# Performance work log

Measured on AMD Instinct MI355X. Metric: run time of the kernel, lower is better.

Reference implementation:

```python
import jax, jax.numpy as jnp
import numpy as np

N_NODES = 100000
D_MODEL = 256
N_SLOTS = 512


def setup_inputs() -> dict:
    key = jax.random.key(0)
    k1, k2, k3 = jax.random.split(key, 3)
    query = jax.random.normal(k1, (N_NODES, D_MODEL), dtype=jnp.float32)
    memory_attr = jax.random.normal(k2, (N_SLOTS, D_MODEL), dtype=jnp.float32)
    memory_struct = jax.random.normal(k3, (N_SLOTS, D_MODEL), dtype=jnp.float32)
    return {"query": query, "memory_attr": memory_attr, "memory_struct": memory_struct}


def _read(mem, query):
    # score: [N, M]; original also computes softmax over dim 0 (score_query)
    # but never uses it, so it has no effect on the output and is omitted.
    score = jnp.matmul(query, mem.T)              # [N, M]
    score_memory = jax.nn.softmax(score, axis=1)  # row-wise addressing weights
    read_memory = jnp.matmul(score_memory, mem)   # [N, D]
    return jnp.concatenate((query, read_memory), axis=1)  # [N, 2D]


def reference(query, memory_attr, memory_struct):
    output_attr = _read(memory_attr, query)
    output_struct = _read(memory_struct, query)
    # stack the two read results: [2, N, 2D]
    return jnp.stack((output_attr, output_struct), axis=0)
```

## Files before the change

### kernel.cpp

```cpp
#include <hip/hip_runtime.h>

#define N_ROWS 100000
#define DM 256
#define NS 512

typedef __attribute__((ext_vector_type(8))) short short8;
typedef __attribute__((ext_vector_type(4))) float floatx4;

__device__ __forceinline__ unsigned short f2bf(float x) {
  unsigned int u = __float_as_uint(x);
  u += 0x7fff + ((u >> 16) & 1);
  return (unsigned short)(u >> 16);
}
__device__ __forceinline__ float bf2f(unsigned short h) {
  return __uint_as_float(((unsigned int)h) << 16);
}

__global__ __launch_bounds__(256) void prep_split(const float* __restrict__ mA,
                                                  const float* __restrict__ mS,
                                                  unsigned short* __restrict__ ws) {
  const int mem = blockIdx.y;
  const float* M = mem ? mS : mA;
  unsigned short* base = ws + (size_t)mem * 3 * (NS * DM);
  const int t = blockIdx.x * 256 + threadIdx.x;
  const float x = M[t];
  const unsigned short h = f2bf(x);
  const unsigned short l = f2bf(x - bf2f(h));
  base[t] = h;
  base[NS * DM + t] = l;
  const int row = t >> 8;
  const int col = t & (DM - 1);
  base[2 * NS * DM + col * NS + row] = h;
}

__global__ __launch_bounds__(256, 2) void attn_main(
    const float* __restrict__ q,
    const unsigned short* __restrict__ ws,
    float* __restrict__ out) {
  constexpr int PITCH = 40;

  __shared__ unsigned short MhS[256 * PITCH];
  __shared__ unsigned short MlS[256 * PITCH];
  __shared__ unsigned short QhS[64 * PITCH];
  __shared__ unsigned short QlS[64 * PITCH];
  __shared__ unsigned short MtS[256 * PITCH];
  __shared__ unsigned short PS[64 * PITCH];
  __shared__ float redmax[4][64];
  __shared__ float redsum[4][64];

  const int tid = threadIdx.x;
  const int w   = tid >> 6;
  const int l   = tid & 63;
  const int l15 = l & 15;
  const int lq  = l >> 4;
  const int mem = blockIdx.y;
  const int qbase = blockIdx.x * 64;

  const unsigned short* Mh = ws + (size_t)mem * 3 * (NS * DM);
  const unsigned short* Ml = Mh + NS * DM;
  const unsigned short* Mt = Mh + 2 * NS * DM;
  float* outM = out + (size_t)mem * N_ROWS * (2 * DM);

  #pragma unroll
  for (int u = 0; u < 16; ++u) {
    const int idx = u * 256 + tid;
    const int row = idx >> 6, c4 = idx & 63;
    const int grow = qbase + row;
    if (grow < N_ROWS) {
      const float4 v = *(const float4*)(q + (size_t)grow * DM + c4 * 4);
      *(float4*)(outM + (size_t)grow * (2 * DM) + c4 * 4) = v;
    }
  }

  const int wrow = (w & 1) * 32;
  const int wq   = w >> 1;

  floatx4 acc[2][16];
  #pragma unroll
  for (int rt = 0; rt < 2; ++rt)
    #pragma unroll
    for (int j = 0; j < 16; ++j) acc[rt][j] = (floatx4){0.f, 0.f, 0.f, 0.f};

  for (int kc = 0; kc < 8; ++kc) {
    {
      const int row = tid >> 2, o = tid & 3;
      int grow = qbase + row;
      if (grow >= N_ROWS) grow = N_ROWS - 1;
      const float* src = q + (size_t)grow * DM + kc * 32 + o * 8;
      const float4 a = *(const float4*)src;
      const float4 b = *(const float4*)(src + 4);
      const float xs[8] = {a.x, a.y, a.z, a.w, b.x, b.y, b.z, b.w};
      union { short8 v; unsigned short s[8]; } uh, ul;
      #pragma unroll
      for (int e = 0; e < 8; ++e) {
        const unsigned short hh = f2bf(xs[e]);
        uh.s[e] = hh;
        ul.s[e] = f2bf(xs[e] - bf2f(hh));
      }
      *(short8*)(&QhS[row * PITCH + o * 8]) = uh.v;
      *(short8*)(&QlS[row * PITCH + o * 8]) = ul.v;
    }
    #pragma unroll
    for (int sc = 0; sc < 2; ++sc) {
      #pragma unroll
      for (int u = 0; u < 4; ++u) {
        const int i = u * 256 + tid;
        const int srow = i >> 2, o = i & 3;
        const size_t goff = (size_t)(sc * 256 + srow) * DM + kc * 32 + o * 8;
        *(short8*)(&MhS[srow * PITCH + o * 8]) = *(const short8*)(Mh + goff);
        *(short8*)(&MlS[srow * PITCH + o * 8]) = *(const short8*)(Ml + goff);
      }
      __syncthreads();
      short8 ah[2], al[2];
      #pragma unroll
      for (int rt = 0; rt < 2; ++rt) {
        const int row = wrow + rt * 16 + l15;
        ah[rt] = *(const short8*)(&QhS[row * PITCH + lq * 8]);
        al[rt] = *(const short8*)(&QlS[row * PITCH + lq * 8]);
      }
      #pragma unroll
      for (int nt = 0; nt < 8; ++nt) {
        const int srow = wq * 128 + nt * 16 + l15;
        const short8 bh = *(const short8*)(&MhS[srow * PITCH + lq * 8]);
        const short8 bl = *(const short8*)(&MlS[srow * PITCH + lq * 8]);
        #pragma unroll
        for (int rt = 0; rt < 2; ++rt) {
          floatx4 c = acc[rt][sc * 8 + nt];
          c = __builtin_amdgcn_mfma_f32_16x16x32_bf16(ah[rt], bh, c, 0, 0, 0);
          c = __builtin_amdgcn_mfma_f32_16x16x32_bf16(ah[rt], bl, c, 0, 0, 0);
          c = __builtin_amdgcn_mfma_f32_16x16x32_bf16(al[rt], bh, c, 0, 0, 0);
          acc[rt][sc * 8 + nt] = c;
        }
      }
      __syncthreads();
    }
  }

  float rowm[2][4], rowinv[2][4];
  {
    float pm[2][4];
    #pragma unroll
    for (int rt = 0; rt < 2; ++rt)
      #pragma unroll
      for (int r = 0; r < 4; ++r) {
        float m = -1e30f;
        #pragma unroll
        for (int j = 0; j < 16; ++j) m = fmaxf(m, acc[rt][j][r]);
        pm[rt][r] = m;
      }
    #pragma unroll
    for (int off = 1; off <= 8; off <<= 1)
      #pragma unroll
      for (int rt = 0; rt < 2; ++rt)
        #pragma unroll
        for (int r = 0; r < 4; ++r)
          pm[rt][r] = fmaxf(pm[rt][r], __shfl_xor(pm[rt][r], off));
    if (l15 == 0) {
      #pragma unroll
      for (int rt = 0; rt < 2; ++rt)
        #pragma unroll
        for (int r = 0; r < 4; ++r)
          redmax[w][wrow + rt * 16 + lq * 4 + r] = pm[rt][r];
    }
    __syncthreads();
    #pragma unroll
    for (int rt = 0; rt < 2; ++rt)
      #pragma unroll
      for (int r = 0; r < 4; ++r) {
        const int row = wrow + rt * 16 + lq * 4 + r;
        rowm[rt][r] = fmaxf(redmax[w][row], redmax[w ^ 2][row]);
      }
    float psum[2][4] = {{0.f, 0.f, 0.f, 0.f}, {0.f, 0.f, 0.f, 0.f}};
    #pragma unroll
    for (int rt = 0; rt < 2; ++rt)
      #pragma unroll
      for (int j = 0; j < 16; ++j) {
        floatx4 c = acc[rt][j];
        #pragma unroll
        for (int r = 0; r < 4; ++r) {
          const float e = __expf(c[r] - rowm[rt][r]);
          c[r] = e;
          psum[rt][r] += e;
        }
        acc[rt][j] = c;
      }
    #pragma unroll
    for (int off = 1; off <= 8; off <<= 1)
      #pragma unroll
      for (int rt = 0; rt < 2; ++rt)
        #pragma unroll
        for (int r = 0; r < 4; ++r)
          psum[rt][r] += __shfl_xor(psum[rt][r], off);
    if (l15 == 0) {
      #pragma unroll
      for (int rt = 0; rt < 2; ++rt)
        #pragma unroll
        for (int r = 0; r < 4; ++r)
          redsum[w][wrow + rt * 16 + lq * 4 + r] = psum[rt][r];
    }
    __syncthreads();
    #pragma unroll
    for (int rt = 0; rt < 2; ++rt)
      #pragma unroll
      for (int r = 0; r < 4; ++r) {
        const int row = wrow + rt * 16 + lq * 4 + r;
        rowinv[rt][r] = 1.f / (redsum[w][row] + redsum[w ^ 2][row]);
      }
  }

  floatx4 oacc[4][4];
  #pragma unroll
  for (int mt = 0; mt < 4; ++mt)
    #pragma unroll
    for (int nt = 0; nt < 4; ++nt) oacc[mt][nt] = (floatx4){0.f, 0.f, 0.f, 0.f};

  #pragma unroll
  for (int kc2 = 0; kc2 < 16; ++kc2) {
    #pragma unroll
    for (int u = 0; u < 4; ++u) {
      const int i = u * 256 + tid;
      const int drow = i >> 2, o = i & 3;
      *(short8*)(&MtS[drow * PITCH + o * 8]) =
          *(const short8*)(Mt + (size_t)drow * NS + kc2 * 32 + o * 8);
    }
    if (wq == ((kc2 >> 2) & 1)) {
      const int sc  = kc2 >> 3;
      const int nt0 = (kc2 & 3) * 2;
      #pragma unroll
      for (int nn = 0; nn < 2; ++nn)
        #pragma unroll
        for (int rt = 0; rt < 2; ++rt) {
          const floatx4 c = acc[rt][sc * 8 + nt0 + nn];
          #pragma unroll
          for (int r = 0; r < 4; ++r) {
            const unsigned short pb = f2bf(c[r] * rowinv[rt][r]);
            PS[(wrow + rt * 16 + lq * 4 + r) * PITCH + nn * 16 + l15] = pb;
          }
        }
    }
    __syncthreads();
    short8 bfr[4];
    #pragma unroll
    for (int nt = 0; nt < 4; ++nt)
      bfr[nt] = *(const short8*)(&PS[(nt * 16 + l15) * PITCH + lq * 8]);
    #pragma unroll
    for (int mt = 0; mt < 4; ++mt) {
      const int drow = w * 64 + mt * 16 + l15;
      const short8 a = *(const short8*)(&MtS[drow * PITCH + lq * 8]);
      #pragma unroll
      for (int nt = 0; nt < 4; ++nt)
        oacc[mt][nt] =
            __builtin_amdgcn_mfma_f32_16x16x32_bf16(a, bfr[nt], oacc[mt][nt], 0, 0, 0);
    }
    __syncthreads();
  }

  #pragma unroll
  for (int mt = 0; mt < 4; ++mt)
    #pragma unroll
    for (int nt = 0; nt < 4; ++nt) {
      const int grow = qbase + nt * 16 + l15;
      if (grow < N_ROWS) {
        const int d0 = w * 64 + mt * 16 + lq * 4;
        *(floatx4*)(outM + (size_t)grow * (2 * DM) + DM + d0) = oacc[mt][nt];
      }
    }
}

extern "C" void kernel_launch(void* const* d_in, const int* in_sizes, int n_in,
                              void* d_out, int out_size, void* d_ws, size_t ws_size,
                              hipStream_t stream) {
  const float* query = (const float*)d_in[0];
  const float* mA    = (const float*)d_in[1];
  const float* mS    = (const float*)d_in[2];
  float* out = (float*)d_out;
  unsigned short* ws = (unsigned short*)d_ws;

  hipLaunchKernelGGL(prep_split, dim3(512, 2), dim3(256), 0, stream, mA, mS, ws);
  hipLaunchKernelGGL(attn_main, dim3((N_ROWS + 63) / 64, 2), dim3(256), 0, stream,
                     query, ws, out);
}
```

Measured before the change: 793.3 us.

## Double-buffer memory tiles via async global-to-LDS loads with swizzled layout

Pre-tiles the split bf16 memory arrays in the prep kernel into swizzled 32-column tiles so the main kernel can stream them into LDS with global_load_lds DMA. The tiles are double-buffered so the next tile's load overlaps the current MFMA work. The query copy to the output is interleaved with the K loop, and the P/Mt stage is software-pipelined. An XOR swizzle replaces the padded pitch to avoid LDS bank conflicts, and s_setprio is raised around MFMA blocks. In exchange there are more LDS-layout assumptions and a subtler barrier/ordering scheme for the async loads.

```diff
diff --git a/kernel.cpp b/kernel.cpp
--- a/kernel.cpp
+++ b/kernel.cpp
@@ -14,6 +14,10 @@
 }
 __device__ __forceinline__ float bf2f(unsigned short h) {
   return __uint_as_float(((unsigned int)h) << 16);
+}
+
+__device__ __forceinline__ int swz(int row, int col16) {
+  return row * 4 + (col16 ^ ((row >> 1) & 3));
 }
 
 __global__ __launch_bounds__(256) void prep_split(const float* __restrict__ mA,
@@ -26,25 +30,43 @@
   const float x = M[t];
   const unsigned short h = f2bf(x);
   const unsigned short l = f2bf(x - bf2f(h));
-  base[t] = h;
-  base[NS * DM + t] = l;
-  const int row = t >> 8;
-  const int col = t & (DM - 1);
-  base[2 * NS * DM + col * NS + row] = h;
+  const int slot = t >> 8;
+  const int d = t & (DM - 1);
+  {
+    const int kc = d >> 5, c = d & 31;
+    const int sc = slot >> 8, srow = slot & 255;
+    const int tile = kc * 2 + sc;
+    const int g = swz(srow, c >> 3);
+    base[tile * 8192 + g * 8 + (c & 7)] = h;
+    base[NS * DM + tile * 8192 + g * 8 + (c & 7)] = l;
+  }
+  {
+    const int kc2 = slot >> 5, cs = slot & 31;
+    const int g = swz(d, cs >> 3);
+    base[2 * NS * DM + kc2 * 8192 + g * 8 + (cs & 7)] = h;
+  }
+}
+
+__device__ __forceinline__ void async16(const void* g, void* l) {
+  typedef const __attribute__((address_space(1))) unsigned int GU;
+  typedef __attribute__((address_space(3))) unsigned int LU;
+  __builtin_amdgcn_global_load_lds((GU*)g, (LU*)l, 16, 0, 0);
+}
+
+__device__ __forceinline__ void dma_tile(const unsigned short* __restrict__ g,
+                                         unsigned short* l, int tid) {
+  unsigned short* lw = l + (tid >> 6) * 512;
+  const unsigned short* gp = g + tid * 8;
+  #pragma unroll
+  for (int r = 0; r < 4; ++r)
+    async16(gp + r * 2048, lw + r * 2048);
 }
 
 __global__ __launch_bounds__(256, 2) void attn_main(
     const float* __restrict__ q,
     const unsigned short* __restrict__ ws,
     float* __restrict__ out) {
-  constexpr int PITCH = 40;
-
-  __shared__ unsigned short MhS[256 * PITCH];
-  __shared__ unsigned short MlS[256 * PITCH];
-  __shared__ unsigned short QhS[64 * PITCH];
-  __shared__ unsigned short QlS[64 * PITCH];
-  __shared__ unsigned short MtS[256 * PITCH];
-  __shared__ unsigned short PS[64 * PITCH];
+  __shared__ __align__(16) unsigned short sm[36864];
   __shared__ float redmax[4][64];
   __shared__ float redsum[4][64];
 
@@ -55,84 +77,117 @@
   const int lq  = l >> 4;
   const int mem = blockIdx.y;
   const int qbase = blockIdx.x * 64;
-
-  const unsigned short* Mh = ws + (size_t)mem * 3 * (NS * DM);
-  const unsigned short* Ml = Mh + NS * DM;
-  const unsigned short* Mt = Mh + 2 * NS * DM;
-  float* outM = out + (size_t)mem * N_ROWS * (2 * DM);
-
-  #pragma unroll
-  for (int u = 0; u < 16; ++u) {
-    const int idx = u * 256 + tid;
-    const int row = idx >> 6, c4 = idx & 63;
-    const int grow = qbase + row;
-    if (grow < N_ROWS) {
-      const float4 v = *(const float4*)(q + (size_t)grow * DM + c4 * 4);
-      *(float4*)(outM + (size_t)grow * (2 * DM) + c4 * 4) = v;
-    }
-  }
-
   const int wrow = (w & 1) * 32;
   const int wq   = w >> 1;
 
+  const unsigned short* MhT = ws + (size_t)mem * 3 * (NS * DM);
+  const unsigned short* MlT = MhT + NS * DM;
+  const unsigned short* MtT = MhT + 2 * NS * DM;
+  float* outM = out + (size_t)mem * N_ROWS * (2 * DM);
+
+  auto issue_m = [&](int j) {
+    dma_tile(MhT + j * 8192, sm + (j & 1) * 16384, tid);
+    dma_tile(MlT + j * 8192, sm + (j & 1) * 16384 + 8192, tid);
+  };
+  auto issue_mt = [&](int j) {
+    dma_tile(MtT + j * 8192, sm + (j & 1) * 8192, tid);
+  };
+
+  float4 qa, qb;
+  auto load_q = [&](int kc) {
+    int grow = qbase + (tid >> 2);
+    if (grow >= N_ROWS) grow = N_ROWS - 1;
+    const float* src = q + (size_t)grow * DM + kc * 32 + (tid & 3) * 8;
+    qa = *(const float4*)src;
+    qb = *(const float4*)(src + 4);
+  };
+  auto split_write_q = [&]() {
+    const int row = tid >> 2, o = tid & 3;
+    const float xs[8] = {qa.x, qa.y, qa.z, qa.w, qb.x, qb.y, qb.z, qb.w};
+    union { short8 v; unsigned short s[8]; } uh, ul;
+    #pragma unroll
+    for (int e = 0; e < 8; ++e) {
+      const unsigned short hh = f2bf(xs[e]);
+      uh.s[e] = hh;
+      ul.s[e] = f2bf(xs[e] - bf2f(hh));
+    }
+    const int g = swz(row, o);
+    *(short8*)(sm + 32768 + g * 8) = uh.v;
+    *(short8*)(sm + 34816 + g * 8) = ul.v;
+  };
+  auto store_qcopy = [&](int kc) {
+    const int grow = qbase + (tid >> 2);
+    if (grow < N_ROWS) {
+      float* dst = outM + (size_t)grow * (2 * DM) + kc * 32 + (tid & 3) * 8;
+      *(float4*)dst = qa;
+      *(float4*)(dst + 4) = qb;
+    }
+  };
+
   floatx4 acc[2][16];
   #pragma unroll
   for (int rt = 0; rt < 2; ++rt)
     #pragma unroll
     for (int j = 0; j < 16; ++j) acc[rt][j] = (floatx4){0.f, 0.f, 0.f, 0.f};
 
+  load_q(0);
+  issue_m(0);
+  __syncthreads();
+  split_write_q();
+  __syncthreads();
+  issue_m(1);
+  store_qcopy(0);
+  load_q(1);
+
   for (int kc = 0; kc < 8; ++kc) {
-    {
-      const int row = tid >> 2, o = tid & 3;
-      int grow = qbase + row;
-      if (grow >= N_ROWS) grow = N_ROWS - 1;
-      const float* src = q + (size_t)grow * DM + kc * 32 + o * 8;
-      const float4 a = *(const float4*)src;
-      const float4 b = *(const float4*)(src + 4);
-      const float xs[8] = {a.x, a.y, a.z, a.w, b.x, b.y, b.z, b.w};
-      union { short8 v; unsigned short s[8]; } uh, ul;
-      #pragma unroll
-      for (int e = 0; e < 8; ++e) {
-        const unsigned short hh = f2bf(xs[e]);
-        uh.s[e] = hh;
-        ul.s[e] = f2bf(xs[e] - bf2f(hh));
-      }
-      *(short8*)(&QhS[row * PITCH + o * 8]) = uh.v;
-      *(short8*)(&QlS[row * PITCH + o * 8]) = ul.v;
-    }
-    #pragma unroll
-    for (int sc = 0; sc < 2; ++sc) {
-      #pragma unroll
-      for (int u = 0; u < 4; ++u) {
-        const int i = u * 256 + tid;
-        const int srow = i >> 2, o = i & 3;
-        const size_t goff = (size_t)(sc * 256 + srow) * DM + kc * 32 + o * 8;
-        *(short8*)(&MhS[srow * PITCH + o * 8]) = *(const short8*)(Mh + goff);
-        *(short8*)(&MlS[srow * PITCH + o * 8]) = *(const short8*)(Ml + goff);
-      }
+    short8 ah[2], al[2];
+    #pragma unroll
+    for (int rt = 0; rt < 2; ++rt) {
+      const int g = swz(wrow + rt * 16 + l15, lq);
+      ah[rt] = *(const short8*)(sm + 32768 + g * 8);
+      al[rt] = *(const short8*)(sm + 34816 + g * 8);
+    }
+    __builtin_amdgcn_s_setprio(1);
+    #pragma unroll
+    for (int nt = 0; nt < 8; ++nt) {
+      const int g = swz(wq * 128 + nt * 16 + l15, lq);
+      const short8 bh = *(const short8*)(sm + g * 8);
+      const short8 bl = *(const short8*)(sm + 8192 + g * 8);
+      #pragma unroll
+      for (int rt = 0; rt < 2; ++rt) {
+        floatx4 c = acc[rt][nt];
+        c = __builtin_amdgcn_mfma_f32_16x16x32_bf16(ah[rt], bh, c, 0, 0, 0);
+        c = __builtin_amdgcn_mfma_f32_16x16x32_bf16(ah[rt], bl, c, 0, 0, 0);
+        c = __builtin_amdgcn_mfma_f32_16x16x32_bf16(al[rt], bh, c, 0, 0, 0);
+        acc[rt][nt] = c;
+      }
+    }
+    __builtin_amdgcn_s_setprio(0);
+    __syncthreads();
+    if (kc < 7) issue_m(2 * kc + 2);
+    __builtin_amdgcn_s_setprio(1);
+    #pragma unroll
+    for (int nt = 0; nt < 8; ++nt) {
+      const int g = swz(wq * 128 + nt * 16 + l15, lq);
+      const short8 bh = *(const short8*)(sm + 16384 + g * 8);
+      const short8 bl = *(const short8*)(sm + 24576 + g * 8);
+      #pragma unroll
+      for (int rt = 0; rt < 2; ++rt) {
+        floatx4 c = acc[rt][8 + nt];
+        c = __builtin_amdgcn_mfma_f32_16x16x32_bf16(ah[rt], bh, c, 0, 0, 0);
+        c = __builtin_amdgcn_mfma_f32_16x16x32_bf16(ah[rt], bl, c, 0, 0, 0);
+        c = __builtin_amdgcn_mfma_f32_16x16x32_bf16(al[rt], bh, c, 0, 0, 0);
+        acc[rt][8 + nt] = c;
+      }
+    }
+    __builtin_amdgcn_s_setprio(0);
+    if (kc < 7) {
       __syncthreads();
-      short8 ah[2], al[2];
-      #pragma unroll
-      for (int rt = 0; rt < 2; ++rt) {
-        const int row = wrow + rt * 16 + l15;
-        ah[rt] = *(const short8*)(&QhS[row * PITCH + lq * 8]);
-        al[rt] = *(const short8*)(&QlS[row * PITCH + lq * 8]);
-      }
-      #pragma unroll
-      for (int nt = 0; nt < 8; ++nt) {
-        const int srow = wq * 128 + nt * 16 + l15;
-        const short8 bh = *(const short8*)(&MhS[srow * PITCH + lq * 8]);
-        const short8 bl = *(const short8*)(&MlS[srow * PITCH + lq * 8]);
-        #pragma unroll
-        for (int rt = 0; rt < 2; ++rt) {
-          floatx4 c = acc[rt][sc * 8 + nt];
-          c = __builtin_amdgcn_mfma_f32_16x16x32_bf16(ah[rt], bh, c, 0, 0, 0);
-          c = __builtin_amdgcn_mfma_f32_16x16x32_bf16(ah[rt], bl, c, 0, 0, 0);
-          c = __builtin_amdgcn_mfma_f32_16x16x32_bf16(al[rt], bh, c, 0, 0, 0);
-          acc[rt][sc * 8 + nt] = c;
-        }
-      }
+      split_write_q();
       __syncthreads();
+      issue_m(2 * kc + 3);
+      store_qcopy(kc + 1);
+      if (kc < 6) load_q(kc + 2);
     }
   }
 
@@ -163,6 +218,8 @@
           redmax[w][wrow + rt * 16 + lq * 4 + r] = pm[rt][r];
     }
     __syncthreads();
+    issue_mt(0);
+    issue_mt(1);
     #pragma unroll
     for (int rt = 0; rt < 2; ++rt)
       #pragma unroll
@@ -214,45 +271,47 @@
     #pragma unroll
     for (int nt = 0; nt < 4; ++nt) oacc[mt][nt] = (floatx4){0.f, 0.f, 0.f, 0.f};
 
+  auto write_ps = [&](int c) {
+    const int scp = c >> 3, nt0 = (c & 3) * 2;
+    const int b = 32768 + (c & 1) * 2048;
+    #pragma unroll
+    for (int nn = 0; nn < 2; ++nn)
+      #pragma unroll
+      for (int rt = 0; rt < 2; ++rt) {
+        const floatx4 v = acc[rt][scp * 8 + nt0 + nn];
+        #pragma unroll
+        for (int r = 0; r < 4; ++r) {
+          const int row = wrow + rt * 16 + lq * 4 + r;
+          const int col = nn * 16 + l15;
+          sm[b + swz(row, col >> 3) * 8 + (col & 7)] =
+              f2bf(v[r] * rowinv[rt][r]);
+        }
+      }
+  };
+
+  if (wq == 0) write_ps(0);
+  __syncthreads();
   #pragma unroll
   for (int kc2 = 0; kc2 < 16; ++kc2) {
-    #pragma unroll
-    for (int u = 0; u < 4; ++u) {
-      const int i = u * 256 + tid;
-      const int drow = i >> 2, o = i & 3;
-      *(short8*)(&MtS[drow * PITCH + o * 8]) =
-          *(const short8*)(Mt + (size_t)drow * NS + kc2 * 32 + o * 8);
-    }
-    if (wq == ((kc2 >> 2) & 1)) {
-      const int sc  = kc2 >> 3;
-      const int nt0 = (kc2 & 3) * 2;
-      #pragma unroll
-      for (int nn = 0; nn < 2; ++nn)
-        #pragma unroll
-        for (int rt = 0; rt < 2; ++rt) {
-          const floatx4 c = acc[rt][sc * 8 + nt0 + nn];
-          #pragma unroll
-          for (int r = 0; r < 4; ++r) {
-            const unsigned short pb = f2bf(c[r] * rowinv[rt][r]);
-            PS[(wrow + rt * 16 + lq * 4 + r) * PITCH + nn * 16 + l15] = pb;
-          }
-        }
-    }
-    __syncthreads();
+    const unsigned short* mtb = sm + (kc2 & 1) * 8192;
+    const unsigned short* ps  = sm + 32768 + (kc2 & 1) * 2048;
     short8 bfr[4];
     #pragma unroll
     for (int nt = 0; nt < 4; ++nt)
-      bfr[nt] = *(const short8*)(&PS[(nt * 16 + l15) * PITCH + lq * 8]);
+      bfr[nt] = *(const short8*)(ps + swz(nt * 16 + l15, lq) * 8);
+    __builtin_amdgcn_s_setprio(1);
     #pragma unroll
     for (int mt = 0; mt < 4; ++mt) {
-      const int drow = w * 64 + mt * 16 + l15;
-      const short8 a = *(const short8*)(&MtS[drow * PITCH + lq * 8]);
+      const short8 a = *(const short8*)(mtb + swz(w * 64 + mt * 16 + l15, lq) * 8);
       #pragma unroll
       for (int nt = 0; nt < 4; ++nt)
         oacc[mt][nt] =
             __builtin_amdgcn_mfma_f32_16x16x32_bf16(a, bfr[nt], oacc[mt][nt], 0, 0, 0);
     }
+    __builtin_amdgcn_s_setprio(0);
+    if (kc2 < 15 && wq == (((kc2 + 1) >> 2) & 1)) write_ps(kc2 + 1);
     __syncthreads();
+    if (kc2 < 14) issue_mt(kc2 + 2);
   }
 
   #pragma unroll
```

After: 713.5 us. 10.1% less time.
